# Performance work log

Hardware: AMD Instinct MI355X
Metric: run time of the kernel (lower is better)

## Reference

```python
import math
import jax, jax.numpy as jnp
import numpy as np
from jax import lax

RADIUS = 3
KSIZE = 2 * RADIUS + 1  # 7
TOP_K = 8
SINKHORN_ITERS = 5


def _box_sum(x, h_axis, w_axis):
    # sum pooling with same padding over spatial axes
    wd = [1] * x.ndim
    wd[h_axis] = KSIZE
    wd[w_axis] = KSIZE
    pads = [(0, 0)] * x.ndim
    pads[h_axis] = (RADIUS, RADIUS)
    pads[w_axis] = (RADIUS, RADIUS)
    return lax.reduce_window(x, 0.0, lax.add, tuple(wd), (1,) * x.ndim, pads)


def geo_validate(src_pos, cand_pos, H, W):
    # src_pos [B,N,2], cand_pos [B,N,K,2] -> score [B,N,K]
    B, N, K, _ = cand_pos.shape
    src = src_pos.reshape(B, H, W, 1, 2)
    cand = cand_pos.reshape(B, H, W, K, 2)
    disp = cand - src  # [B,H,W,K,2]
    # count_include_pad=False -> divide by number of valid (in-bounds) taps
    cnt = _box_sum(jnp.ones((1, H, W, 1, 1), disp.dtype), 1, 2)
    mean = _box_sum(disp, 1, 2) / cnt
    mean_sq = _box_sum(disp * disp, 1, 2) / cnt
    var = jnp.clip(mean_sq - mean * mean, 0.0)
    total_var = var.sum(-1).reshape(B, N, K)
    return 1.0 / (1.0 + 100.0 * total_var)


def optimal_transport(scores, dustbin):
    B, M, N = scores.shape
    row = jnp.broadcast_to(dustbin, (B, M, 1))
    col = jnp.broadcast_to(dustbin, (B, 1, N))
    corner = jnp.zeros((B, 1, 1), scores.dtype)
    Z = jnp.concatenate([jnp.concatenate([scores, row], 2),
                         jnp.concatenate([col, corner], 2)], 1)  # [B,M+1,N+1]
    norm = -math.log(M + N)
    log_mu = jnp.full((M + 1,), norm, scores.dtype).at[M].set(math.log(N) + norm)
    log_nu = jnp.full((N + 1,), norm, scores.dtype).at[N].set(math.log(M) + norm)
    log_mu = jnp.broadcast_to(log_mu, (B, M + 1))
    log_nu = jnp.broadcast_to(log_nu, (B, N + 1))

    def body(_, uv):
        u, v = uv
        u = log_mu - jax.nn.logsumexp(Z + v[:, None, :], axis=2)
        v = log_nu - jax.nn.logsumexp(Z + u[:, :, None], axis=1)
        return (u, v)

    u0 = jnp.zeros((B, M + 1), scores.dtype)
    v0 = jnp.zeros((B, N + 1), scores.dtype)
    u, v = lax.fori_loop(0, SINKHORN_ITERS, body, (u0, v0))
    log_assign = Z + u[:, :, None] + v[:, None, :]
    return log_assign[:, :M, :N]


def solve_weighted_affine(src_pts, dst_pts, weights):
    # src/dst [B,N,2], weights [B,N,1] -> H_mat [B,3,3]
    B, N, _ = src_pts.shape
    w = weights[..., 0]
    w = w / jnp.clip(w.sum(1, keepdims=True), 1e-6)
    x, y = src_pts[..., 0], src_pts[..., 1]
    one = jnp.ones_like(x)
    zero = jnp.zeros_like(x)
    row_x = jnp.stack([x, y, one, zero, zero, zero], -1)   # [B,N,6]
    row_y = jnp.stack([zero, zero, zero, x, y, one], -1)
    A = jnp.concatenate([row_x, row_y], 1)                 # [B,2N,6]
    b = jnp.concatenate([dst_pts[..., 0], dst_pts[..., 1]], 1)[..., None]
    wd = jnp.concatenate([w, w], 1)[..., None]             # [B,2N,1]
    Aw = A * wd
    AtWA = jnp.einsum('bni,bnj->bij', Aw, A) + 1e-4 * jnp.eye(6, dtype=A.dtype)
    AtWb = jnp.einsum('bni,bnk->bik', Aw, b)
    p = jnp.linalg.solve(AtWA, AtWb)[..., 0]               # [B,6]
    a_, b_, c_, d_, e_, f_ = [p[:, i] for i in range(6)]
    z = jnp.zeros_like(a_)
    o = jnp.ones_like(a_)
    return jnp.stack([a_, b_, c_, d_, e_, f_, z, z, o], -1).reshape(B, 3, 3)


def matcher_forward(feat_A, feat_B, pos_A, pos_B, dustbin_score, geo_weight,
                    current_temp, H, W):
    B, N, C = feat_A.shape
    temp = current_temp[0]
    nA = feat_A / jnp.clip(jnp.linalg.norm(feat_A, axis=-1, keepdims=True), 1e-12)
    nB = feat_B / jnp.clip(jnp.linalg.norm(feat_B, axis=-1, keepdims=True), 1e-12)
    scores = jnp.einsum('bnc,bmc->bnm', nA, nB) / temp      # [B,N,N]
    log_assign = optimal_transport(scores, dustbin_score[0])
    ot_prob = jnp.exp(log_assign)
    topk_vals, topk_idx = lax.top_k(ot_prob, TOP_K)          # [B,N,K]
    bidx = jnp.arange(B)[:, None, None]
    topk_pos = pos_B[bidx, topk_idx]                         # [B,N,K,2]
    geo = geo_validate(pos_A, topk_pos, H, W)                # [B,N,K]
    gw = jnp.clip(geo_weight[0], 0.0, 2.0)
    combined = topk_vals + gw * geo
    soft = jax.nn.softmax(combined / temp, axis=-1)
    refined_warp = (topk_pos * soft[..., None]).sum(2)       # [B,N,2]
    conf = (soft * topk_vals).sum(-1, keepdims=True)         # [B,N,1]
    H_mat = solve_weighted_affine(pos_A, refined_warp, conf)
    return refined_warp, conf, H_mat


def setup_inputs() -> dict:
    key = jax.random.key(0)
    kA, kB, kP = jax.random.split(key, 3)
    B, H, W, C = 2, 64, 64, 128
    N = H * W
    feat_A = jax.random.normal(kA, (B, N, C), jnp.float32)
    feat_B = jax.random.normal(kB, (B, N, C), jnp.float32)
    # dense grid positions, normalized to [0,1]
    ys, xs = jnp.meshgrid(jnp.arange(H, dtype=jnp.float32),
                          jnp.arange(W, dtype=jnp.float32), indexing='ij')
    grid = jnp.stack([xs, ys], -1).reshape(1, N, 2) / float(max(H, W))
    pos_A = jnp.broadcast_to(grid, (B, N, 2))
    pos_B = pos_A + 0.01 * jax.random.normal(kP, (B, N, 2), jnp.float32)
    return {
        'feat_A': feat_A, 'feat_B': feat_B,
        'pos_A': pos_A, 'pos_B': pos_B,
        'dustbin_score': jnp.full((1,), -1.0, jnp.float32),
        'geo_weight': jnp.full((1,), 0.5, jnp.float32),
        'current_temp': jnp.full((1,), 0.1, jnp.float32),
        'H': H, 'W': W,
    }


def reference(feat_A, feat_B, pos_A, pos_B, dustbin_score, geo_weight,
              current_temp, H, W):
    return matcher_forward(feat_A, feat_B, pos_A, pos_B, dustbin_score,
                           geo_weight, current_temp, H, W)
```

## Files before the change

### kernel.cpp

```cpp
#include <hip/hip_runtime.h>
#include <math.h>

#define UVS 4104

#define OFF_ZU    33554432ul
#define OFF_WV    (OFF_ZU + 2*UVS)
#define OFF_RN    (OFF_WV + 2*UVS)
#define OFF_PARTS (OFF_RN + 16384)
#define OFF_TKV   (OFF_PARTS + 2097152)
#define OFF_TKP   (OFF_TKV + 65536)
#define OFF_DP    (OFF_TKP + 131072)
#define OFF_GEO   (OFF_DP + 131072)
#define OFF_SUM   (OFF_GEO + 65536)

#define EXPC    0.0001220703125f
#define HALFC   0.5f

typedef __attribute__((ext_vector_type(8))) short bf16x8;
typedef __attribute__((ext_vector_type(4))) float f32x4;

static __device__ __forceinline__ unsigned f2bf(float x) {
    unsigned u = __float_as_uint(x);
    return (u + 0x7FFFu + ((u >> 16) & 1u)) >> 16;
}
static __device__ __forceinline__ float bf2f(unsigned h) { return __uint_as_float(h << 16); }

static __device__ __forceinline__ unsigned long long shfl_xor_u64(unsigned long long v, int m) {
    unsigned lo = (unsigned)v, hi = (unsigned)(v >> 32);
    lo = __shfl_xor(lo, m, 64);
    hi = __shfl_xor(hi, m, 64);
    return ((unsigned long long)hi << 32) | lo;
}

__global__ __launch_bounds__(256) void init_kernel(float* __restrict__ wv)
{
    int i = blockIdx.x * 256 + threadIdx.x;
    if (i < 2 * UVS) wv[i] = 1.0f;
}

__global__ __launch_bounds__(256) void norms_kernel(
    const float* __restrict__ fA, const float* __restrict__ fB, float* __restrict__ rn)
{
    int t = threadIdx.x;
    int rowg = blockIdx.x * 4 + (t >> 6);
    int lane = t & 63;
    const float* f = (rowg < 8192) ? fA : fB;
    int r = rowg & 8191;
    float x0 = f[(size_t)r * 128 + lane];
    float x1 = f[(size_t)r * 128 + 64 + lane];
    float s = x0 * x0 + x1 * x1;
    #pragma unroll
    for (int off = 32; off > 0; off >>= 1) s += __shfl_xor(s, off, 64);
    if (lane == 0) rn[rowg] = 1.f / fmaxf(sqrtf(s), 1e-12f);
}

#define LDK 72
__global__ __launch_bounds__(256) void gemm_mfma(
    const float* __restrict__ fA, const float* __restrict__ fB,
    const float* __restrict__ rn, const float* __restrict__ temp,
    float* __restrict__ E0)
{
    __shared__ short Ahi[64 * LDK], Alo[64 * LDK], Bhi[64 * LDK], Blo[64 * LDK];
    int b = blockIdx.z;
    int i0 = blockIdx.y * 64, j0 = blockIdx.x * 64;
    int t = threadIdx.x;
    int r = t >> 2;
    int c0 = (t & 3) * 16;
    int wave = t >> 6, lane = t & 63;
    int fr = lane & 15;
    int quad = lane >> 4;
    f32x4 acc[4] = {f32x4{0,0,0,0}, f32x4{0,0,0,0}, f32x4{0,0,0,0}, f32x4{0,0,0,0}};

    const float* pa0 = fA + ((size_t)(b * 4096 + i0 + r)) * 128 + c0;
    const float* pb0 = fB + ((size_t)(b * 4096 + j0 + r)) * 128 + c0;

    for (int ks = 0; ks < 2; ks++) {
        float4 a4[4], b4[4];
        #pragma unroll
        for (int q = 0; q < 4; q++) {
            a4[q] = *(const float4*)(pa0 + ks * 64 + q * 4);
            b4[q] = *(const float4*)(pb0 + ks * 64 + q * 4);
        }
        __syncthreads();
        #pragma unroll
        for (int q = 0; q < 4; q++) {
            float xv[4] = {a4[q].x, a4[q].y, a4[q].z, a4[q].w};
            unsigned h[4], l[4];
            #pragma unroll
            for (int e = 0; e < 4; e++) { h[e] = f2bf(xv[e]); l[e] = f2bf(xv[e] - bf2f(h[e])); }
            *(uint2*)&Ahi[r * LDK + c0 + q * 4] = make_uint2(h[0] | (h[1] << 16), h[2] | (h[3] << 16));
            *(uint2*)&Alo[r * LDK + c0 + q * 4] = make_uint2(l[0] | (l[1] << 16), l[2] | (l[3] << 16));
            float yv[4] = {b4[q].x, b4[q].y, b4[q].z, b4[q].w};
            #pragma unroll
            for (int e = 0; e < 4; e++) { h[e] = f2bf(yv[e]); l[e] = f2bf(yv[e] - bf2f(h[e])); }
            *(uint2*)&Bhi[r * LDK + c0 + q * 4] = make_uint2(h[0] | (h[1] << 16), h[2] | (h[3] << 16));
            *(uint2*)&Blo[r * LDK + c0 + q * 4] = make_uint2(l[0] | (l[1] << 16), l[2] | (l[3] << 16));
        }
        __syncthreads();
        #pragma unroll
        for (int kk = 0; kk < 2; kk++) {
            int koff = kk * 32 + quad * 8;
            bf16x8 ah = *(const bf16x8*)&Ahi[(wave * 16 + fr) * LDK + koff];
            bf16x8 al = *(const bf16x8*)&Alo[(wave * 16 + fr) * LDK + koff];
            #pragma unroll
            for (int nb = 0; nb < 4; nb++) {
                bf16x8 bh = *(const bf16x8*)&Bhi[(nb * 16 + fr) * LDK + koff];
                bf16x8 bl = *(const bf16x8*)&Blo[(nb * 16 + fr) * LDK + koff];
                acc[nb] = __builtin_amdgcn_mfma_f32_16x16x32_bf16(ah, bh, acc[nb], 0, 0, 0);
                acc[nb] = __builtin_amdgcn_mfma_f32_16x16x32_bf16(al, bh, acc[nb], 0, 0, 0);
                acc[nb] = __builtin_amdgcn_mfma_f32_16x16x32_bf16(ah, bl, acc[nb], 0, 0, 0);
            }
        }
    }
    float invt = 1.f / temp[0];
    int m0 = i0 + wave * 16 + quad * 4;
    float ra[4];
    #pragma unroll
    for (int rr = 0; rr < 4; rr++) ra[rr] = rn[b * 4096 + m0 + rr] * invt;
    #pragma unroll
    for (int nb = 0; nb < 4; nb++) {
        int col = j0 + nb * 16 + fr;
        float rbv = rn[8192 + b * 4096 + col];
        #pragma unroll
        for (int rr = 0; rr < 4; rr++)
            E0[((size_t)(b * 4096 + m0 + rr)) * 4096 + col] = __expf(acc[nb][rr] * (ra[rr] * rbv));
    }
}

__global__ __launch_bounds__(256) void sink_fused(
    const float* __restrict__ E0, float* __restrict__ zu, const float* __restrict__ wv,
    const float* __restrict__ dbp, float* __restrict__ parts)
{
    int b = blockIdx.z;
    int ch = blockIdx.x;
    int t = threadIdx.x;
    int wave = t >> 6, lane = t & 63;
    const float* wb = wv + b * UVS;
    float edb = __expf(dbp[0]);
    __shared__ float Sch[4 * 4096];
    __shared__ float z4[4];

    if (ch == 0) {
        __shared__ float red[256];
        float sv = 0.f;
        #pragma unroll
        for (int k = 0; k < 16; k++) sv += wb[t + k * 256];
        red[t] = sv; __syncthreads();
        for (int off = 128; off > 0; off >>= 1) {
            if (t < off) red[t] += red[t + off];
            __syncthreads();
        }
        if (t == 0) zu[b * UVS + 4096] = HALFC / (edb * red[0] + wb[4096]);
        __syncthreads();
    }

    float dtail = edb * wb[4096];
    float colacc[16];
    #pragma unroll
    for (int k = 0; k < 16; k++) colacc[k] = 0.f;

    const float* Eb = E0 + (size_t)b * 4096 * 4096;

    for (int st = 0; st < 4; st++) {
        int row = ch * 16 + st * 4 + wave;
        const float* Erow = Eb + (size_t)row * 4096;
        float rs = 0.f;
        #pragma unroll
        for (int c = 0; c < 16; c++) {
            int j = lane * 4 + c * 256;
            float4 x = *(const float4*)(Erow + j);
            float4 w = *(const float4*)(wb + j);
            float4 q = make_float4(x.x * w.x, x.y * w.y, x.z * w.z, x.w * w.w);
            *(float4*)&Sch[wave * 4096 + j] = q;
            rs += (q.x + q.y) + (q.z + q.w);
        }
        #pragma unroll
        for (int off = 32; off > 0; off >>= 1) rs += __shfl_xor(rs, off, 64);
        if (lane == 0) {
            float zi = EXPC / (rs + dtail);
            zu[b * UVS + row] = zi;
            z4[wave] = zi;
        }
        __syncthreads();
        float z0 = z4[0], z1 = z4[1], z2 = z4[2], z3 = z4[3];
        #pragma unroll
        for (int k = 0; k < 16; k++) {
            int c = t + k * 256;
            colacc[k] += Sch[c] * z0 + Sch[4096 + c] * z1
                       + Sch[8192 + c] * z2 + Sch[12288 + c] * z3;
        }
        __syncthreads();
    }
    float* pp = parts + ((size_t)(b * 256 + ch)) * 4096;
    #pragma unroll
    for (int k = 0; k < 16; k++) pp[t + k * 256] = colacc[k];
}

__global__ __launch_bounds__(256) void sink_vB(
    const float* __restrict__ parts, const float* __restrict__ zu,
    float* __restrict__ wv, const float* __restrict__ dbp)
{
    int b = blockIdx.z;
    int t = threadIdx.x;
    float edb = __expf(dbp[0]);
    if (blockIdx.x < 16) {
        int j = blockIdx.x * 256 + t;
        float s = 0.f;
        #pragma unroll 16
        for (int ch = 0; ch < 256; ch++) s += parts[((size_t)(b * 256 + ch)) * 4096 + j];
        float wold = wv[b * UVS + j];
        float total = s / wold + edb * zu[b * UVS + 4096];
        wv[b * UVS + j] = EXPC / total;
    } else {
        __shared__ float red[256];
        float s = 0.f;
        for (int i = t; i < 4096; i += 256) s += zu[b * UVS + i];
        red[t] = s; __syncthreads();
        for (int off = 128; off > 0; off >>= 1) {
            if (t < off) red[t] += red[t + off];
            __syncthreads();
        }
        if (t == 0)
            wv[b * UVS + 4096] = HALFC / (edb * red[0] + zu[b * UVS + 4096]);
    }
}

#define CMPSWAP(a, b) { unsigned long long _mx = (a) > (b) ? (a) : (b); \
                        unsigned long long _mn = (a) > (b) ? (b) : (a); \
                        (a) = _mx; (b) = _mn; }
#define FCMPSWAP(a, b) { float _mx = fmaxf(a, b), _mn = fminf(a, b); (a) = _mx; (b) = _mn; }
__global__ __launch_bounds__(256) void topk_kernel(
    const float* __restrict__ E0, const float* __restrict__ zu, const float* __restrict__ wv,
    const float* __restrict__ posA, const float* __restrict__ posB,
    float* __restrict__ tkv, float* __restrict__ tkp, float* __restrict__ dp)
{
    int wave = threadIdx.x >> 6;
    int lane = threadIdx.x & 63;
    int row = blockIdx.x * 4 + wave;
    int b = row >> 12; int i = row & 4095;
    const float* Erow = E0 + (size_t)row * 4096;
    const float* wb = wv + b * UVS;

    __shared__ unsigned long long cand[4][64];
    __shared__ int ccnt[4];
    if (lane == 0) ccnt[wave] = 0;

    float4 q[16];
    float s[8] = {0, 0, 0, 0, 0, 0, 0, 0};
    #pragma unroll
    for (int c = 0; c < 16; c++) {
        int j = c * 256 + lane * 4;
        float4 x = *(const float4*)(Erow + j);
        float4 w = *(const float4*)(wb + j);
        q[c] = make_float4(x.x * w.x, x.y * w.y, x.z * w.z, x.w * w.w);
        float el[4] = {q[c].x, q[c].y, q[c].z, q[c].w};
        #pragma unroll
        for (int e = 0; e < 4; e++) {
            float xv = el[e];
            #pragma unroll
            for (int rr = 0; rr < 8; rr++) {
                float mx = fmaxf(s[rr], xv);
                float mn = fminf(s[rr], xv);
                s[rr] = mx; xv = mn;
            }
        }
    }

    #pragma unroll
    for (int st = 0; st < 6; st++) {
        int off = 1 << st;
        float o[8];
        #pragma unroll
        for (int r = 0; r < 8; r++) o[r] = __shfl_xor(s[r], off, 64);
        float m[8];
        #pragma unroll
        for (int r = 0; r < 8; r++) m[r] = fmaxf(s[r], o[7 - r]);
        FCMPSWAP(m[0], m[4]); FCMPSWAP(m[1], m[5]); FCMPSWAP(m[2], m[6]); FCMPSWAP(m[3], m[7]);
        FCMPSWAP(m[0], m[2]); FCMPSWAP(m[1], m[3]); FCMPSWAP(m[4], m[6]); FCMPSWAP(m[5], m[7]);
        FCMPSWAP(m[0], m[1]); FCMPSWAP(m[2], m[3]); FCMPSWAP(m[4], m[5]); FCMPSWAP(m[6], m[7]);
        #pragma unroll
        for (int r = 0; r < 8; r++) s[r] = m[r];
    }
    float t8 = s[7];

    __syncthreads();

    #pragma unroll
    for (int c = 0; c < 16; c++) {
        float el[4] = {q[c].x, q[c].y, q[c].z, q[c].w};
        #pragma unroll
        for (int e = 0; e < 4; e++) {
            if (el[e] >= t8) {
                int j = c * 256 + lane * 4 + e;
                unsigned long long key =
                    ((unsigned long long)__float_as_uint(el[e]) << 32) | (unsigned)(4095 - j);
                int slot = atomicAdd(&ccnt[wave], 1);
                if (slot < 64) cand[wave][slot] = key;
            }
        }
    }
    __syncthreads();

    int cnt = ccnt[wave]; if (cnt > 64) cnt = 64;
    unsigned long long loc[8];
    loc[0] = (lane < cnt) ? cand[wave][lane] : 0ull;
    #pragma unroll
    for (int r = 1; r < 8; r++) loc[r] = 0ull;
    #pragma unroll
    for (int st = 0; st < 6; st++) {
        int off = 1 << st;
        unsigned long long oth[8];
        #pragma unroll
        for (int r = 0; r < 8; r++) oth[r] = shfl_xor_u64(loc[r], off);
        unsigned long long m[8];
        #pragma unroll
        for (int r = 0; r < 8; r++) {
            unsigned long long a = loc[r], bb = oth[7 - r];
            m[r] = a > bb ? a : bb;
        }
        CMPSWAP(m[0], m[4]); CMPSWAP(m[1], m[5]); CMPSWAP(m[2], m[6]); CMPSWAP(m[3], m[7]);
        CMPSWAP(m[0], m[2]); CMPSWAP(m[1], m[3]); CMPSWAP(m[4], m[6]); CMPSWAP(m[5], m[7]);
        CMPSWAP(m[0], m[1]); CMPSWAP(m[2], m[3]); CMPSWAP(m[4], m[5]); CMPSWAP(m[6], m[7]);
        #pragma unroll
        for (int r = 0; r < 8; r++) loc[r] = m[r];
    }

    if (lane < 8) {
        unsigned long long key = loc[0];
        #pragma unroll
        for (int r = 1; r < 8; r++) if (lane == r) key = loc[r];
        int idx = 4095 - (int)(key & 0xFFFFFFFFu);
        float candv = __uint_as_float((unsigned)(key >> 32));
        float val = candv * zu[b * UVS + i];
        float px = posB[((size_t)(b * 4096 + idx)) * 2 + 0];
        float py = posB[((size_t)(b * 4096 + idx)) * 2 + 1];
        float ax = posA[((size_t)(b * 4096 + i)) * 2 + 0];
        float ay = posA[((size_t)(b * 4096 + i)) * 2 + 1];
        size_t base = ((size_t)(b * 4096 + i)) * 8 + lane;
        tkv[base] = val;
        tkp[base * 2 + 0] = px; tkp[base * 2 + 1] = py;
        dp[((size_t)((b * 8 + lane) * 2 + 0)) * 4096 + i] = px - ax;
        dp[((size_t)((b * 8 + lane) * 2 + 1)) * 4096 + i] = py - ay;
    }
}

__global__ __launch_bounds__(256) void geo_kernel(
    const float* __restrict__ dp, float* __restrict__ geo)
{
    int tid = blockIdx.x * 256 + threadIdx.x;
    int n = tid & 4095; int bk = tid >> 12;
    int b = bk >> 3; int k = bk & 7;
    int h = n >> 6, w = n & 63;
    const float* dpx = dp + ((size_t)(bk * 2 + 0)) * 4096;
    const float* dpy = dp + ((size_t)(bk * 2 + 1)) * 4096;
    float sx = 0, sy = 0, sxx = 0, syy = 0, cnt = 0;
    #pragma unroll
    for (int dy = -3; dy <= 3; dy++) {
        int hh = h + dy; if ((unsigned)hh >= 64u) continue;
        #pragma unroll
        for (int dx = -3; dx <= 3; dx++) {
            int ww = w + dx; if ((unsigned)ww >= 64u) continue;
            int nn = (hh << 6) + ww;
            float vx = dpx[nn], vy = dpy[nn];
            sx += vx; sy += vy; sxx += vx * vx; syy += vy * vy; cnt += 1.f;
        }
    }
    float inv = 1.f / cnt;
    float mx = sx * inv, my = sy * inv;
    float varx = fmaxf(sxx * inv - mx * mx, 0.f);
    float vary = fmaxf(syy * inv - my * my, 0.f);
    geo[((size_t)(b * 4096 + n)) * 8 + k] = 1.f / (1.f + 100.f * (varx + vary));
}

__global__ __launch_bounds__(256) void refine_kernel(
    const float* __restrict__ tkv, const float* __restrict__ geo,
    const float* __restrict__ tkp, const float* __restrict__ gwp,
    const float* __restrict__ tpp, float* __restrict__ out)
{
    int tid = blockIdx.x * 256 + threadIdx.x;
    float gw = fminf(fmaxf(gwp[0], 0.f), 2.f);
    float invt = 1.f / tpp[0];
    size_t base = (size_t)tid * 8;
    float cb[8], vv[8];
    float mx = -INFINITY;
    #pragma unroll
    for (int k = 0; k < 8; k++) { vv[k] = tkv[base + k]; cb[k] = vv[k] + gw * geo[base + k]; mx = fmaxf(mx, cb[k]); }
    float e[8], se = 0;
    #pragma unroll
    for (int k = 0; k < 8; k++) { e[k] = __expf((cb[k] - mx) * invt); se += e[k]; }
    float wx = 0, wy = 0, cf = 0; float inv = 1.f / se;
    #pragma unroll
    for (int k = 0; k < 8; k++) {
        float s = e[k] * inv;
        wx += s * tkp[(base + k) * 2 + 0];
        wy += s * tkp[(base + k) * 2 + 1];
        cf += s * vv[k];
    }
    out[(size_t)tid * 2 + 0] = wx;
    out[(size_t)tid * 2 + 1] = wy;
    out[16384 + tid] = cf;
}

__global__ __launch_bounds__(256) void affine_reduce(
    const float* __restrict__ posA, const float* __restrict__ out, double* __restrict__ sums)
{
    int b = blockIdx.x; int t = threadIdx.x;
    double acc[12] = {0,0,0,0,0,0,0,0,0,0,0,0};
    for (int n = t; n < 4096; n += 256) {
        size_t idx = (size_t)b * 4096 + n;
        float x = posA[idx * 2], y = posA[idx * 2 + 1];
        float dx = out[idx * 2], dy = out[idx * 2 + 1];
        float c = out[16384 + idx];
        double cd = (double)c;
        double cx = cd * x, cy = cd * y;
        acc[0] += cx * x;  acc[1] += cx * y;  acc[2] += cy * y;
        acc[3] += cx;      acc[4] += cy;      acc[5] += cd;
        acc[6] += cx * dx; acc[7] += cy * dx; acc[8] += cd * dx;
        acc[9] += cx * dy; acc[10] += cy * dy; acc[11] += cd * dy;
    }
    __shared__ double red[256];
    for (int s = 0; s < 12; s++) {
        red[t] = acc[s]; __syncthreads();
        for (int off = 128; off > 0; off >>= 1) {
            if (t < off) red[t] += red[t + off];
            __syncthreads();
        }
        if (t == 0) sums[b * 12 + s] = red[0];
        __syncthreads();
    }
}

__global__ void affine_solve(const double* __restrict__ sums, float* __restrict__ out)
{
    int t = threadIdx.x;
    if (t >= 2) return;
    int b = t;
    const double* s = sums + b * 12;
    double den = s[5] > 1e-6 ? s[5] : 1e-6;
    double g00 = s[0] / den + 1e-4, g01 = s[1] / den, g02 = s[3] / den;
    double g11 = s[2] / den + 1e-4, g12 = s[4] / den;
    double g22 = s[5] / den + 1e-4;
    double bx0 = s[6] / den, bx1 = s[7] / den, bx2 = s[8] / den;
    double by0 = s[9] / den, by1 = s[10] / den, by2 = s[11] / den;
    double c00 = g11 * g22 - g12 * g12;
    double c01 = g02 * g12 - g01 * g22;
    double c02 = g01 * g12 - g02 * g11;
    double det = g00 * c00 + g01 * c01 + g02 * c02;
    double id = 1.0 / det;
    double i00 = c00 * id, i01 = c01 * id, i02 = c02 * id;
    double i11 = (g00 * g22 - g02 * g02) * id, i12 = (g01 * g02 - g00 * g12) * id;
    double i22 = (g00 * g11 - g01 * g01) * id;
    double a_ = i00 * bx0 + i01 * bx1 + i02 * bx2;
    double b_ = i01 * bx0 + i11 * bx1 + i12 * bx2;
    double c_ = i02 * bx0 + i12 * bx1 + i22 * bx2;
    double d_ = i00 * by0 + i01 * by1 + i02 * by2;
    double e_ = i01 * by0 + i11 * by1 + i12 * by2;
    double f_ = i02 * by0 + i12 * by1 + i22 * by2;
    float* o = out + 24576 + b * 9;
    o[0] = (float)a_; o[1] = (float)b_; o[2] = (float)c_;
    o[3] = (float)d_; o[4] = (float)e_; o[5] = (float)f_;
    o[6] = 0.f; o[7] = 0.f; o[8] = 1.f;
}

extern "C" void kernel_launch(void* const* d_in, const int* in_sizes, int n_in,
                              void* d_out, int out_size, void* d_ws, size_t ws_size,
                              hipStream_t stream) {
    const float* fA = (const float*)d_in[0];
    const float* fB = (const float*)d_in[1];
    const float* pA = (const float*)d_in[2];
    const float* pB = (const float*)d_in[3];
    const float* db = (const float*)d_in[4];
    const float* gw = (const float*)d_in[5];
    const float* tp = (const float*)d_in[6];

    float* ws    = (float*)d_ws;
    float* out   = (float*)d_out;
    float* E0    = ws;
    float* zu    = ws + OFF_ZU;
    float* wv    = ws + OFF_WV;
    float* rn    = ws + OFF_RN;
    float* parts = ws + OFF_PARTS;
    float* tkv   = ws + OFF_TKV;
    float* tkp   = ws + OFF_TKP;
    float* dp    = ws + OFF_DP;
    float* geo   = ws + OFF_GEO;
    double* sums = (double*)(ws + OFF_SUM);

    init_kernel<<<33, 256, 0, stream>>>(wv);
    norms_kernel<<<4096, 256, 0, stream>>>(fA, fB, rn);
    gemm_mfma<<<dim3(64, 64, 2), 256, 0, stream>>>(fA, fB, rn, tp, E0);

    for (int it = 0; it < 5; it++) {
        sink_fused<<<dim3(256, 1, 2), 256, 0, stream>>>(E0, zu, wv, db, parts);
        sink_vB<<<dim3(17, 1, 2), 256, 0, stream>>>(parts, zu, wv, db);
    }

    topk_kernel<<<2048, 256, 0, stream>>>(E0, zu, wv, pA, pB, tkv, tkp, dp);
    geo_kernel<<<256, 256, 0, stream>>>(dp, geo);
    refine_kernel<<<32, 256, 0, stream>>>(tkv, geo, tkp, gw, tp, out);
    affine_reduce<<<2, 256, 0, stream>>>(pA, out, sums);
    affine_solve<<<1, 64, 0, stream>>>(sums, out);
}
```

Baseline: 390.1 us.

## Pre-pack features into MFMA-ready bf16 hi/lo planes before the GEMM

Adds a pack kernel that splits each fp32 feature into bf16 hi and lo parts once, writing them in an MFMA fragment-ordered layout into reused workspace (the parts buffer). The GEMM then loads A fragments straight into registers and copies B tiles into shared memory with plain vector loads, over the full K of 128 in one pass. This removes the repeated per-block fp32-to-bf16 conversion and the two-stage shared-memory restaging, at the cost of one extra launch and an extra read and write of the packed data.

```diff
diff --git a/kernel.cpp b/kernel.cpp
--- a/kernel.cpp
+++ b/kernel.cpp
@@ -16,6 +16,8 @@
 #define EXPC    0.0001220703125f
 #define HALFC   0.5f
 
+#define PLANE   1048576
+
 typedef __attribute__((ext_vector_type(8))) short bf16x8;
 typedef __attribute__((ext_vector_type(4))) float f32x4;
 
@@ -54,64 +56,79 @@
     if (lane == 0) rn[rowg] = 1.f / fmaxf(sqrtf(s), 1e-12f);
 }
 
-#define LDK 72
+__global__ __launch_bounds__(256) void pack_kernel(
+    const float* __restrict__ fA, const float* __restrict__ fB, short* __restrict__ pk)
+{
+    int gt = blockIdx.x * 256 + threadIdx.x;
+    int tensor = gt >> 17;
+    int t = gt & 131071;
+    int fr = t & 15;
+    int kc = (t >> 4) & 15;
+    int rb = (t >> 8) & 255;
+    int b  = t >> 16;
+    const float* src = tensor ? fB : fA;
+    const float* p = src + ((size_t)(b * 4096 + rb * 16 + fr)) * 128 + kc * 8;
+    float4 v0 = *(const float4*)p;
+    float4 v1 = *(const float4*)(p + 4);
+    float el[8] = {v0.x, v0.y, v0.z, v0.w, v1.x, v1.y, v1.z, v1.w};
+    unsigned h[8], l[8];
+    #pragma unroll
+    for (int e = 0; e < 8; e++) { h[e] = f2bf(el[e]); l[e] = f2bf(el[e] - bf2f(h[e])); }
+    uint4 hw = make_uint4(h[0] | (h[1] << 16), h[2] | (h[3] << 16),
+                          h[4] | (h[5] << 16), h[6] | (h[7] << 16));
+    uint4 lw = make_uint4(l[0] | (l[1] << 16), l[2] | (l[3] << 16),
+                          l[4] | (l[5] << 16), l[6] | (l[7] << 16));
+    size_t off = ((size_t)(b * 256 + rb)) * 2048 + kc * 128 + fr * 8;
+    short* hi = pk + (size_t)tensor * 2 * PLANE;
+    *(uint4*)(hi + off) = hw;
+    *(uint4*)(hi + PLANE + off) = lw;
+}
+
 __global__ __launch_bounds__(256) void gemm_mfma(
-    const float* __restrict__ fA, const float* __restrict__ fB,
-    const float* __restrict__ rn, const float* __restrict__ temp,
-    float* __restrict__ E0)
-{
-    __shared__ short Ahi[64 * LDK], Alo[64 * LDK], Bhi[64 * LDK], Blo[64 * LDK];
+    const short* __restrict__ pk, const float* __restrict__ rn,
+    const float* __restrict__ temp, float* __restrict__ E0)
+{
+    __shared__ short Bs[16384];
     int b = blockIdx.z;
     int i0 = blockIdx.y * 64, j0 = blockIdx.x * 64;
     int t = threadIdx.x;
-    int r = t >> 2;
-    int c0 = (t & 3) * 16;
     int wave = t >> 6, lane = t & 63;
     int fr = lane & 15;
     int quad = lane >> 4;
+
+    const short* gBhi = pk + 2 * (size_t)PLANE + ((size_t)(b * 256 + (j0 >> 4))) * 2048;
+    const short* gBlo = gBhi + PLANE;
+    #pragma unroll
+    for (int c = 0; c < 4; c++) {
+        int ch = c * 256 + t;
+        *(uint4*)&Bs[ch * 8]        = *(const uint4*)(gBhi + ch * 8);
+        *(uint4*)&Bs[8192 + ch * 8] = *(const uint4*)(gBlo + ch * 8);
+    }
+
+    const short* Abase_hi = pk + ((size_t)(b * 256 + (i0 >> 4) + wave)) * 2048;
+    const short* Abase_lo = Abase_hi + PLANE;
+    bf16x8 ah[4], al[4];
+    #pragma unroll
+    for (int s = 0; s < 4; s++) {
+        ah[s] = *(const bf16x8*)(Abase_hi + s * 512 + lane * 8);
+        al[s] = *(const bf16x8*)(Abase_lo + s * 512 + lane * 8);
+    }
+    __syncthreads();
+
     f32x4 acc[4] = {f32x4{0,0,0,0}, f32x4{0,0,0,0}, f32x4{0,0,0,0}, f32x4{0,0,0,0}};
-
-    const float* pa0 = fA + ((size_t)(b * 4096 + i0 + r)) * 128 + c0;
-    const float* pb0 = fB + ((size_t)(b * 4096 + j0 + r)) * 128 + c0;
-
-    for (int ks = 0; ks < 2; ks++) {
-        float4 a4[4], b4[4];
-        #pragma unroll
-        for (int q = 0; q < 4; q++) {
-            a4[q] = *(const float4*)(pa0 + ks * 64 + q * 4);
-            b4[q] = *(const float4*)(pb0 + ks * 64 + q * 4);
-        }
-        __syncthreads();
-        #pragma unroll
-        for (int q = 0; q < 4; q++) {
-            float xv[4] = {a4[q].x, a4[q].y, a4[q].z, a4[q].w};
-            unsigned h[4], l[4];
-            #pragma unroll
-            for (int e = 0; e < 4; e++) { h[e] = f2bf(xv[e]); l[e] = f2bf(xv[e] - bf2f(h[e])); }
-            *(uint2*)&Ahi[r * LDK + c0 + q * 4] = make_uint2(h[0] | (h[1] << 16), h[2] | (h[3] << 16));
-            *(uint2*)&Alo[r * LDK + c0 + q * 4] = make_uint2(l[0] | (l[1] << 16), l[2] | (l[3] << 16));
-            float yv[4] = {b4[q].x, b4[q].y, b4[q].z, b4[q].w};
-            #pragma unroll
-            for (int e = 0; e < 4; e++) { h[e] = f2bf(yv[e]); l[e] = f2bf(yv[e] - bf2f(h[e])); }
-            *(uint2*)&Bhi[r * LDK + c0 + q * 4] = make_uint2(h[0] | (h[1] << 16), h[2] | (h[3] << 16));
-            *(uint2*)&Blo[r * LDK + c0 + q * 4] = make_uint2(l[0] | (l[1] << 16), l[2] | (l[3] << 16));
-        }
-        __syncthreads();
-        #pragma unroll
-        for (int kk = 0; kk < 2; kk++) {
-            int koff = kk * 32 + quad * 8;
-            bf16x8 ah = *(const bf16x8*)&Ahi[(wave * 16 + fr) * LDK + koff];
-            bf16x8 al = *(const bf16x8*)&Alo[(wave * 16 + fr) * LDK + koff];
-            #pragma unroll
-            for (int nb = 0; nb < 4; nb++) {
-                bf16x8 bh = *(const bf16x8*)&Bhi[(nb * 16 + fr) * LDK + koff];
-                bf16x8 bl = *(const bf16x8*)&Blo[(nb * 16 + fr) * LDK + koff];
-                acc[nb] = __builtin_amdgcn_mfma_f32_16x16x32_bf16(ah, bh, acc[nb], 0, 0, 0);
-                acc[nb] = __builtin_amdgcn_mfma_f32_16x16x32_bf16(al, bh, acc[nb], 0, 0, 0);
-                acc[nb] = __builtin_amdgcn_mfma_f32_16x16x32_bf16(ah, bl, acc[nb], 0, 0, 0);
-            }
-        }
-    }
+    #pragma unroll
+    for (int s = 0; s < 4; s++) {
+        int lo = s * 512 + lane * 8;
+        #pragma unroll
+        for (int nb = 0; nb < 4; nb++) {
+            bf16x8 bh = *(const bf16x8*)&Bs[nb * 2048 + lo];
+            bf16x8 bl = *(const bf16x8*)&Bs[8192 + nb * 2048 + lo];
+            acc[nb] = __builtin_amdgcn_mfma_f32_16x16x32_bf16(ah[s], bh, acc[nb], 0, 0, 0);
+            acc[nb] = __builtin_amdgcn_mfma_f32_16x16x32_bf16(al[s], bh, acc[nb], 0, 0, 0);
+            acc[nb] = __builtin_amdgcn_mfma_f32_16x16x32_bf16(ah[s], bl, acc[nb], 0, 0, 0);
+        }
+    }
+
     float invt = 1.f / temp[0];
     int m0 = i0 + wave * 16 + quad * 4;
     float ra[4];
@@ -480,6 +497,7 @@
     float* wv    = ws + OFF_WV;
     float* rn    = ws + OFF_RN;
     float* parts = ws + OFF_PARTS;
+    short* pk    = (short*)(ws + OFF_PARTS);
     float* tkv   = ws + OFF_TKV;
     float* tkp   = ws + OFF_TKP;
     float* dp    = ws + OFF_DP;
@@ -488,7 +506,8 @@
 
     init_kernel<<<33, 256, 0, stream>>>(wv);
     norms_kernel<<<4096, 256, 0, stream>>>(fA, fB, rn);
-    gemm_mfma<<<dim3(64, 64, 2), 256, 0, stream>>>(fA, fB, rn, tp, E0);
+    pack_kernel<<<1024, 256, 0, stream>>>(fA, fB, pk);
+    gemm_mfma<<<dim3(64, 64, 2), 256, 0, stream>>>(pk, rn, tp, E0);
 
     for (int it = 0; it < 5; it++) {
         sink_fused<<<dim3(256, 1, 2), 256, 0, stream>>>(E0, zu, wv, db, parts);
```

Result: faster. 368.7 us (-5.5%).
